# Performance work log

Hardware: AMD Instinct MI355X
Metric: run time of the kernel (lower is better)

The kernel has to match this reference:

```python
import jax, jax.numpy as jnp
import numpy as np
from jax import lax

HIDDEN = 1024; HEADS = 16; HEAD = 64; LAYERS = 4; MLP = 4096
PATCH = 16; TUBE = 2; CROP = 224; FRAMES = 16
GRID = CROP // PATCH          # 14
DEPTH = FRAMES // TUBE        # 8
N_TOK = DEPTH * GRID * GRID   # 1568
EPS = 1e-6
D_ROT = 2 * ((HEAD // 3) // 2)  # 20 per rotary axis (d, h, w); 4 dims left unrotated


def setup_inputs() -> dict:
    key = jax.random.key(0)
    ks = jax.random.split(key, 12)
    w = lambda k, shape: jax.random.normal(k, shape, jnp.float32) * 0.02
    L, H, M = LAYERS, HIDDEN, MLP
    return {
        "pixel_values_videos": jax.random.normal(ks[0], (2, FRAMES, 3, CROP, CROP), jnp.float32),
        "patch_w": w(ks[1], (H, 3, TUBE, PATCH, PATCH)),  # Conv3d OIDHW
        "patch_b": jnp.zeros((H,), jnp.float32),
        "ln1_g": jnp.ones((L, H), jnp.float32), "ln1_b": jnp.zeros((L, H), jnp.float32),
        "qw": w(ks[2], (L, H, H)), "qb": jnp.zeros((L, H), jnp.float32),
        "kw": w(ks[3], (L, H, H)), "kb": jnp.zeros((L, H), jnp.float32),
        "vw": w(ks[4], (L, H, H)), "vb": jnp.zeros((L, H), jnp.float32),
        "pw": w(ks[5], (L, H, H)), "pb": jnp.zeros((L, H), jnp.float32),
        "ln2_g": jnp.ones((L, H), jnp.float32), "ln2_b": jnp.zeros((L, H), jnp.float32),
        "fc1w": w(ks[6], (L, M, H)), "fc1b": jnp.zeros((L, M), jnp.float32),
        "fc2w": w(ks[7], (L, H, M)), "fc2b": jnp.zeros((L, H), jnp.float32),
        "lnf_g": jnp.ones((H,), jnp.float32), "lnf_b": jnp.zeros((H,), jnp.float32),
    }


def _layer_norm(x, g, b):
    mu = jnp.mean(x, axis=-1, keepdims=True)
    var = jnp.mean(jnp.square(x - mu), axis=-1, keepdims=True)
    return (x - mu) * lax.rsqrt(var + EPS) * g + b


def _position_ids():
    ids = jnp.arange(N_TOK)
    tpf = GRID * GRID
    d_pos = ids // tpf
    rem = ids - d_pos * tpf
    h_pos = rem // GRID
    w_pos = rem - h_pos * GRID
    return d_pos, h_pos, w_pos


def _rotate(x, pos):
    # x: (B, H, N, D); matches VJEPA2 rotate_queries_or_keys:
    # tiled (not interleaved) sin/cos * interleaved rotate-half.
    D = x.shape[-1]
    omega = 1.0 / (10000.0 ** (jnp.arange(D // 2, dtype=x.dtype) / (D / 2.0)))
    freq = pos.astype(x.dtype)[:, None] * omega              # (N, D/2)
    sin = jnp.concatenate([jnp.sin(freq)] * 2, axis=-1)      # (N, D) tiled (torch .repeat)
    cos = jnp.concatenate([jnp.cos(freq)] * 2, axis=-1)
    y = x.reshape(x.shape[:-1] + (D // 2, 2))
    y = jnp.stack([-y[..., 1], y[..., 0]], axis=-1).reshape(x.shape)
    return x * cos + y * sin


def _apply_rope(x, pos_ids):
    d_pos, h_pos, w_pos = pos_ids
    s0, s1, s2 = 0, D_ROT, 2 * D_ROT
    parts = [_rotate(x[..., s0:s1], d_pos), _rotate(x[..., s1:s2], h_pos),
             _rotate(x[..., s2:3 * D_ROT], w_pos)]
    if 3 * D_ROT < HEAD:
        parts.append(x[..., 3 * D_ROT:])
    return jnp.concatenate(parts, axis=-1)


def _forward(pixel_values_videos, patch_w, patch_b, ln1_g, ln1_b, qw, qb, kw, kb,
             vw, vb, pw, pb, ln2_g, ln2_b, fc1w, fc1b, fc2w, fc2b, lnf_g, lnf_b):
    B = pixel_values_videos.shape[0]
    x = jnp.transpose(pixel_values_videos, (0, 2, 1, 3, 4))  # (B, C, T, H, W)
    h = lax.conv_general_dilated(x, patch_w, window_strides=(TUBE, PATCH, PATCH),
                                 padding="VALID",
                                 dimension_numbers=("NCDHW", "OIDHW", "NCDHW"))
    h = h + patch_b[None, :, None, None, None]
    h = h.reshape(B, HIDDEN, -1).transpose(0, 2, 1)          # (B, N, HIDDEN)

    pos_ids = _position_ids()
    scale = HEAD ** -0.5

    for i in range(LAYERS):
        # attention block
        xn = _layer_norm(h, ln1_g[i], ln1_b[i])
        def heads(w_, b_):
            return (xn @ w_.T + b_).reshape(B, N_TOK, HEADS, HEAD).transpose(0, 2, 1, 3)
        q = _apply_rope(heads(qw[i], qb[i]), pos_ids)
        k = _apply_rope(heads(kw[i], kb[i]), pos_ids)
        v = heads(vw[i], vb[i])
        aw = jnp.einsum("bhnd,bhmd->bhnm", q, k) * scale
        aw = jax.nn.softmax(aw.astype(jnp.float32), axis=-1).astype(q.dtype)
        o = jnp.einsum("bhnm,bhmd->bhnd", aw, v)
        o = o.transpose(0, 2, 1, 3).reshape(B, N_TOK, HIDDEN)
        h = h + (o @ pw[i].T + pb[i])
        # MLP block
        xn = _layer_norm(h, ln2_g[i], ln2_b[i])
        m = jax.nn.gelu(xn @ fc1w[i].T + fc1b[i], approximate=False)
        h = h + (m @ fc2w[i].T + fc2b[i])

    return _layer_norm(h, lnf_g, lnf_b)


def reference(pixel_values_videos, patch_w, patch_b, ln1_g, ln1_b, qw, qb, kw, kb,
              vw, vb, pw, pb, ln2_g, ln2_b, fc1w, fc1b, fc2w, fc2b, lnf_g, lnf_b):
    return _forward(pixel_values_videos, patch_w, patch_b, ln1_g, ln1_b, qw, qb, kw, kb,
                    vw, vb, pw, pb, ln2_g, ln2_b, fc1w, fc1b, fc2w, fc2b, lnf_g, lnf_b)
```

## Files before the change

kernel.cpp:

```cpp
#include <hip/hip_runtime.h>
#include <math.h>

#define NTOK   1568
#define BATCH  2
#define HID    1024
#define MLPD   4096
#define NLAYER 4
#define ROWS   (BATCH*NTOK)
#define CONVK  1536

typedef __bf16 bf16x8 __attribute__((ext_vector_type(8)));
typedef __bf16 bf16x2 __attribute__((ext_vector_type(2)));
typedef float  f32x4  __attribute__((ext_vector_type(4)));

__device__ __forceinline__ unsigned short f2b(float f) {
  unsigned int u = __float_as_uint(f);
  unsigned int r = u + 0x7FFFu + ((u >> 16) & 1u);
  return (unsigned short)(r >> 16);
}
__device__ __forceinline__ float b2f(unsigned short s) {
  return __uint_as_float((unsigned int)s << 16);
}
__device__ __forceinline__ unsigned cvt2(float a, float b) {
  bf16x2 t;
  t[0] = (__bf16)a;
  t[1] = (__bf16)b;
  return __builtin_bit_cast(unsigned, t);
}
__device__ __forceinline__ float e2(float x) { return __builtin_amdgcn_exp2f(x); }

__device__ __forceinline__ void async16(const unsigned short* g, unsigned short* l) {
  __builtin_amdgcn_global_load_lds(
      (__attribute__((address_space(1))) void*)(void*)g,
      (__attribute__((address_space(3))) void*)(void*)l, 16, 0, 0);
}

__global__ __launch_bounds__(256) void cast4_k(const float* __restrict__ s,
                                               unsigned short* __restrict__ d,
                                               long long n4) {
  long long i = (long long)blockIdx.x * 256 + threadIdx.x;
  long long stride = (long long)gridDim.x * 256;
  for (; i < n4; i += stride) {
    float4 v = ((const float4*)s)[i];
    *(ushort4*)(d + i * 4) = make_ushort4(f2b(v.x), f2b(v.y), f2b(v.z), f2b(v.w));
  }
}

__global__ __launch_bounds__(256) void castqkv_k(const float* __restrict__ q,
                                                 const float* __restrict__ k,
                                                 const float* __restrict__ v,
                                                 unsigned short* __restrict__ dst) {
  const float* src = blockIdx.y == 0 ? q : (blockIdx.y == 1 ? k : v);
  long long i4 = (long long)blockIdx.x * 256 + threadIdx.x;
  long long e = i4 * 4;
  int layer = (int)(e >> 20);
  long long de = e + ((long long)(2 * layer + blockIdx.y) << 20);
  float4 val = ((const float4*)src)[i4];
  *(ushort4*)(dst + de) = make_ushort4(f2b(val.x), f2b(val.y), f2b(val.z), f2b(val.w));
}

__global__ __launch_bounds__(256) void biascat_k(const float* __restrict__ qb,
                                                 const float* __restrict__ kb,
                                                 const float* __restrict__ vb,
                                                 float* __restrict__ dst) {
  int idx = blockIdx.x * 256 + threadIdx.x;
  int layer = idx / 3072, c = idx % 3072;
  float v = c < 1024 ? qb[layer * 1024 + c]
            : (c < 2048 ? kb[layer * 1024 + c - 1024] : vb[layer * 1024 + c - 2048]);
  dst[idx] = v;
}

__global__ __launch_bounds__(256) void im2col_k(const float* __restrict__ pv,
                                                unsigned short* __restrict__ A) {
  int idx = blockIdx.x * 256 + threadIdx.x;
  int row = idx / CONVK, col = idx % CONVK;
  int b = row / NTOK, t = row % NTOK;
  int d = t / 196, r = t % 196, hh = r / 14, ww = r % 14;
  int c = col >> 9, r2 = col & 511, td = r2 >> 8, ph = (r2 >> 4) & 15, pw = r2 & 15;
  int frame = 2 * d + td;
  const float* src = pv + ((((long long)b * 16 + frame) * 3 + c) * 224 + (hh * 16 + ph)) * 224
                        + (ww * 16 + pw);
  A[idx] = f2b(*src);
}

__global__ __launch_bounds__(256) void gemm_bt(const unsigned short* __restrict__ A,
                                               const unsigned short* __restrict__ B,
                                               unsigned short* outP,
                                               int M, int N, int K, int kChunk,
                                               size_t zStride) {
  __shared__ unsigned short As[2][128 * 32];
  __shared__ unsigned short Bs[2][128 * 32];
  const int tid = threadIdx.x;
  const int lane = tid & 63;
  const int w = tid >> 6;
  const int wm = (w >> 1) * 64, wn = (w & 1) * 64;
  const int l15 = lane & 15, l4 = lane >> 4;
  const int bm = blockIdx.y, bn = blockIdx.x;
  const int wbase = tid & ~63;
  const int kbeg = blockIdx.z * kChunk;

  auto stage = [&](int buf, int k0) {
#pragma unroll
    for (int it = 0; it < 2; ++it) {
      int c = it * 256 + tid;
      int rowA = bm * 128 + (c >> 2);
      if (rowA >= M) rowA = M - 1;
      async16(A + (size_t)rowA * K + k0 + (c & 3) * 8, &As[buf][(it * 256 + wbase) * 8]);
      int rowB = bn * 128 + (c >> 2);
      async16(B + (size_t)rowB * K + k0 + (c & 3) * 8, &Bs[buf][(it * 256 + wbase) * 8]);
    }
  };

  f32x4 acc[4][4] = {};
  stage(0, kbeg);
  const int nIter = kChunk >> 5;

  for (int i = 0; i < nIter; ++i) {
    const int cur = i & 1;
    __syncthreads();
    if (i + 1 < nIter) stage(cur ^ 1, kbeg + (i + 1) * 32);

    bf16x8 af[4], bfr[4];
#pragma unroll
    for (int ii = 0; ii < 4; ++ii)
      af[ii] = *(const bf16x8*)&As[cur][(wm + ii * 16 + l15) * 32 + l4 * 8];
#pragma unroll
    for (int j = 0; j < 4; ++j)
      bfr[j] = *(const bf16x8*)&Bs[cur][(wn + j * 16 + l15) * 32 + l4 * 8];
#pragma unroll
    for (int ii = 0; ii < 4; ++ii)
#pragma unroll
      for (int j = 0; j < 4; ++j)
        acc[ii][j] = __builtin_amdgcn_mfma_f32_16x16x32_bf16(af[ii], bfr[j], acc[ii][j], 0, 0, 0);
  }

  unsigned short* pout = outP + (size_t)blockIdx.z * zStride;
#pragma unroll
  for (int ii = 0; ii < 4; ++ii) {
    int rowb = bm * 128 + wm + ii * 16 + l4 * 4;
#pragma unroll
    for (int r = 0; r < 4; ++r) {
      int rr = rowb + r;
      if (rr >= M) continue;
#pragma unroll
      for (int j = 0; j < 4; ++j) {
        int col = bn * 128 + wn + j * 16 + l15;
        pout[(size_t)rr * N + col] = f2b(acc[ii][j][r]);
      }
    }
  }
}

template <int NP, int GELU>
__global__ __launch_bounds__(256) void reduceN_k(const unsigned short* p,
                                                 const float* __restrict__ bias,
                                                 unsigned short* outB,
                                                 int MN, int N, size_t pStride) {
  int i8 = blockIdx.x * 256 + threadIdx.x;
  int e = i8 * 8;
  float acc[8];
#pragma unroll
  for (int j = 0; j < 8; ++j) acc[j] = 0.0f;
#pragma unroll
  for (int pp = 0; pp < NP; ++pp) {
    const unsigned short* src = p + (size_t)pp * pStride + e;
    ushort4 a0 = *(const ushort4*)src;
    ushort4 a1 = *(const ushort4*)(src + 4);
    acc[0] += b2f(a0.x); acc[1] += b2f(a0.y); acc[2] += b2f(a0.z); acc[3] += b2f(a0.w);
    acc[4] += b2f(a1.x); acc[5] += b2f(a1.y); acc[6] += b2f(a1.z); acc[7] += b2f(a1.w);
  }
  int col = e % N;
  float4 b0 = *(const float4*)(bias + col);
  float4 b1 = *(const float4*)(bias + col + 4);
  acc[0] += b0.x; acc[1] += b0.y; acc[2] += b0.z; acc[3] += b0.w;
  acc[4] += b1.x; acc[5] += b1.y; acc[6] += b1.z; acc[7] += b1.w;
  if (GELU) {
#pragma unroll
    for (int j = 0; j < 8; ++j)
      acc[j] = 0.5f * acc[j] * (1.0f + erff(acc[j] * 0.70710678118654752f));
  }
  *(ushort4*)(outB + e) = make_ushort4(f2b(acc[0]), f2b(acc[1]), f2b(acc[2]), f2b(acc[3]));
  *(ushort4*)(outB + e + 4) = make_ushort4(f2b(acc[4]), f2b(acc[5]), f2b(acc[6]), f2b(acc[7]));
}

template <int NP, int RESID, int FINAL>
__global__ __launch_bounds__(256) void redln_k(const unsigned short* __restrict__ p,
                                               const float* __restrict__ bias,
                                               const float* resid,
                                               const float* __restrict__ g,
                                               const float* __restrict__ b,
                                               float* hOut,
                                               unsigned short* __restrict__ xnOut,
                                               float* __restrict__ fOut,
                                               size_t pStride) {
  __shared__ float red[8];
  const int row = blockIdx.x, tid = threadIdx.x;
  const int col = tid * 4;
  const size_t off = (size_t)row * HID + col;
  float v0 = 0, v1 = 0, v2 = 0, v3 = 0;
#pragma unroll
  for (int pp = 0; pp < NP; ++pp) {
    ushort4 a = *(const ushort4*)(p + (size_t)pp * pStride + off);
    v0 += b2f(a.x); v1 += b2f(a.y); v2 += b2f(a.z); v3 += b2f(a.w);
  }
  float4 bs = *(const float4*)(bias + col);
  v0 += bs.x; v1 += bs.y; v2 += bs.z; v3 += bs.w;
  if (RESID) {
    float4 r = *(const float4*)(resid + off);
    v0 += r.x; v1 += r.y; v2 += r.z; v3 += r.w;
  }
  if (!FINAL) *(float4*)(hOut + off) = make_float4(v0, v1, v2, v3);
  float s = v0 + v1 + v2 + v3;
  float q = v0 * v0 + v1 * v1 + v2 * v2 + v3 * v3;
  for (int o2 = 32; o2; o2 >>= 1) { s += __shfl_xor(s, o2); q += __shfl_xor(q, o2); }
  if ((tid & 63) == 0) { red[tid >> 6] = s; red[4 + (tid >> 6)] = q; }
  __syncthreads();
  float ts = red[0] + red[1] + red[2] + red[3];
  float tq = red[4] + red[5] + red[6] + red[7];
  float mu = ts * (1.0f / HID);
  float var = tq * (1.0f / HID) - mu * mu;
  float rs = rsqrtf(var + 1e-6f);
  float o0 = (v0 - mu) * rs * g[col + 0] + b[col + 0];
  float o1 = (v1 - mu) * rs * g[col + 1] + b[col + 1];
  float o2 = (v2 - mu) * rs * g[col + 2] + b[col + 2];
  float o3 = (v3 - mu) * rs * g[col + 3] + b[col + 3];
  if (FINAL) {
    *(float4*)(fOut + off) = make_float4(o0, o1, o2, o3);
  } else {
    *(ushort4*)(xnOut + off) = make_ushort4(f2b(o0), f2b(o1), f2b(o2), f2b(o3));
  }
}

__global__ __launch_bounds__(256) void qkvprep_k(const unsigned short* __restrict__ qkvb,
                                                 unsigned short* __restrict__ Qh,
                                                 unsigned short* __restrict__ Kh,
                                                 unsigned short* __restrict__ VT) {
  __shared__ unsigned short Vs[64 * 72];
  const int tile = blockIdx.x, bh = blockIdx.y;
  const int b = bh >> 4, head = bh & 15;
  const int tid = threadIdx.x;
  const int tl = tid >> 2, dc = tid & 3;
  const int tg = tile * 64 + tl;
  const int trc = tg < NTOK ? tg : NTOK - 1;
  const bool valid = tg < NTOK;
  const size_t srow = ((size_t)(b * NTOK + trc)) * 3072 + head * 64 + dc * 16;

  {
    uint4 v0 = *(const uint4*)(qkvb + srow + 2048);
    uint4 v1 = *(const uint4*)(qkvb + srow + 2048 + 8);
    *(uint4*)&Vs[tl * 72 + dc * 16] = v0;
    *(uint4*)&Vs[tl * 72 + dc * 16 + 8] = v1;
  }

  const int t = trc;
  const int dpos = t / 196, rem = t - dpos * 196, hpos = rem / 14, wpos = rem - hpos * 14;
  const float LG = 0.9210340371976184f;
  union V16 { uint4 u[2]; unsigned short s[16]; };
  V16 qin, kin, qout, kout;
  qin.u[0] = *(const uint4*)(qkvb + srow);
  qin.u[1] = *(const uint4*)(qkvb + srow + 8);
  kin.u[0] = *(const uint4*)(qkvb + srow + 1024);
  kin.u[1] = *(const uint4*)(qkvb + srow + 1024 + 8);
#pragma unroll
  for (int p = 0; p < 8; ++p) {
    int d0 = dc * 16 + 2 * p;
    float qx0 = b2f(qin.s[2 * p]), qx1 = b2f(qin.s[2 * p + 1]);
    float kx0 = b2f(kin.s[2 * p]), kx1 = b2f(kin.s[2 * p + 1]);
    float qo0, qo1, ko0, ko1;
    if (d0 >= 60) { qo0 = qx0; qo1 = qx1; ko0 = kx0; ko1 = kx1; }
    else {
      int region = d0 / 20;
      int j0 = d0 - region * 20;
      int pos = region == 0 ? dpos : (region == 1 ? hpos : wpos);
      float fp = (float)pos;
      int i0 = j0 % 10, i1 = (j0 + 1) % 10;
      float f0 = expf(-LG * (float)i0) * fp;
      float f1 = expf(-LG * (float)i1) * fp;
      float c0 = cosf(f0), s0 = sinf(f0), c1 = cosf(f1), s1 = sinf(f1);
      qo0 = qx0 * c0 - qx1 * s0; qo1 = qx1 * c1 + qx0 * s1;
      ko0 = kx0 * c0 - kx1 * s0; ko1 = kx1 * c1 + kx0 * s1;
    }
    const float QS = 0.18033688011112042f;
    qout.s[2 * p]     = f2b(qo0 * QS);
    qout.s[2 * p + 1] = f2b(qo1 * QS);
    kout.s[2 * p]     = f2b(ko0);
    kout.s[2 * p + 1] = f2b(ko1);
  }
  if (valid) {
    size_t drow = ((size_t)bh * NTOK + tg) * 64 + dc * 16;
    *(uint4*)(Qh + drow)     = qout.u[0];
    *(uint4*)(Qh + drow + 8) = qout.u[1];
    *(uint4*)(Kh + drow)     = kout.u[0];
    *(uint4*)(Kh + drow + 8) = kout.u[1];
  }
  __syncthreads();
  {
    int d = tid >> 2, tc = tid & 3;
    if (tile * 64 + tc * 16 < NTOK) {
      V16 o;
#pragma unroll
      for (int jj = 0; jj < 16; ++jj) o.s[jj] = Vs[(tc * 16 + jj) * 72 + d];
      unsigned short* dst = VT + ((size_t)bh * 64 + d) * NTOK + tile * 64 + tc * 16;
      *(uint4*)dst = o.u[0];
      *(uint4*)(dst + 8) = o.u[1];
    }
  }
}

__global__ __launch_bounds__(256, 4) void flash5_k(const unsigned short* __restrict__ Qh,
                                                   const unsigned short* __restrict__ Kh,
                                                   const unsigned short* __restrict__ VT,
                                                   unsigned short* __restrict__ Opart,
                                                   float2* __restrict__ ml) {
  __shared__ unsigned short Ks[2][64 * 64];
  __shared__ unsigned short Vs[2][64 * 64];
  const int bh = blockIdx.x, qt = blockIdx.y, kv = blockIdx.z;
  const int kt0 = kv ? 13 : 0, kt1 = kv ? 25 : 13;
  const int tid = threadIdx.x, lane = tid & 63, w = tid >> 6;
  const int l15 = lane & 15, l4 = lane >> 4;
  const size_t hb = (size_t)bh * NTOK * 64;
  const unsigned short* kgp = Kh + hb;
  const unsigned short* vbp = VT + (size_t)bh * 64 * NTOK;

  const int srow0 = w * 8 + (lane >> 3);
  const int scg0  = (lane & 7) ^ (srow0 & 7);
  const int srow1 = srow0 + 32;
  const int scg1  = (lane & 7) ^ (srow1 & 7);

  const int qrow = qt * 64 + w * 16 + l15;
  const int qrc = qrow < NTOK ? qrow : NTOK - 1;
  bf16x8 q0 = *(const bf16x8*)(Qh + hb + (size_t)qrc * 64 + l4 * 8);
  bf16x8 q1 = *(const bf16x8*)(Qh + hb + (size_t)qrc * 64 + 32 + l4 * 8);

  f32x4 oacc[4] = {};
  float m = -1e30f, l = 0.0f;

  {
    const int kc0 = kt0 * 64;
    async16(kgp + (size_t)(kc0 + srow0) * 64 + scg0 * 8, &Ks[0][(size_t)w * 512]);
    async16(kgp + (size_t)(kc0 + srow1) * 64 + scg1 * 8, &Ks[0][(size_t)(w + 4) * 512]);
    async16(vbp + (size_t)srow0 * NTOK + kc0 + scg0 * 8, &Vs[0][(size_t)w * 512]);
    async16(vbp + (size_t)srow1 * NTOK + kc0 + scg1 * 8, &Vs[0][(size_t)(w + 4) * 512]);
  }

  const int h7 = l15 & 7;
  const int p1 = (l4 ^ h7) * 8;
  const int p2 = ((l4 + 4) ^ h7) * 8;

  for (int kt = kt0; kt < kt1; ++kt) {
    const int cur = (kt - kt0) & 1, nxt = cur ^ 1;
    const int kb = kt * 64;
    __syncthreads();

    if (kt + 1 < kt1) {
      const int kn = kb + 64;
      async16(kgp + (size_t)(kn + srow0) * 64 + scg0 * 8, &Ks[nxt][(size_t)w * 512]);
      async16(kgp + (size_t)(kn + srow1) * 64 + scg1 * 8, &Ks[nxt][(size_t)(w + 4) * 512]);
      async16(vbp + (size_t)srow0 * NTOK + kn + scg0 * 8, &Vs[nxt][(size_t)w * 512]);
      async16(vbp + (size_t)srow1 * NTOK + kn + scg1 * 8, &Vs[nxt][(size_t)(w + 4) * 512]);
    }

    bf16x8 kc0[4], kc1[4];
#pragma unroll
    for (int nt = 0; nt < 4; ++nt) {
      const unsigned short* kr = &Ks[cur][(nt * 16 + l15) * 64];
      kc0[nt] = *(const bf16x8*)(kr + p1);
      kc1[nt] = *(const bf16x8*)(kr + p2);
    }
    f32x4 s[4] = {};
    __builtin_amdgcn_s_setprio(1);
#pragma unroll
    for (int nt = 0; nt < 4; ++nt) {
      s[nt] = __builtin_amdgcn_mfma_f32_16x16x32_bf16(kc0[nt], q0, s[nt], 0, 0, 0);
      s[nt] = __builtin_amdgcn_mfma_f32_16x16x32_bf16(kc1[nt], q1, s[nt], 0, 0, 0);
    }
    __builtin_amdgcn_s_setprio(0);
    bf16x8 vf0[4], vf1[4];
#pragma unroll
    for (int dt = 0; dt < 4; ++dt) {
      const unsigned short* vr = &Vs[cur][(dt * 16 + l15) * 64];
      vf0[dt] = *(const bf16x8*)(vr + p1);
      vf1[dt] = *(const bf16x8*)(vr + p2);
    }

    if (kb + 64 > NTOK) {
#pragma unroll
      for (int nt = 0; nt < 4; ++nt)
#pragma unroll
        for (int r = 0; r < 4; ++r)
          if (kb + nt * 16 + l4 * 4 + r >= NTOK) s[nt][r] = -1e30f;
    }
    float rmax = s[0][0];
#pragma unroll
    for (int nt = 0; nt < 4; ++nt)
#pragma unroll
      for (int r = 0; r < 4; ++r) rmax = fmaxf(rmax, s[nt][r]);
    rmax = fmaxf(rmax, __shfl_xor(rmax, 16));
    rmax = fmaxf(rmax, __shfl_xor(rmax, 32));
    if (!__all(rmax - m <= 11.5f)) {
      float mn = fmaxf(m, rmax);
      float alpha = e2(m - mn);
      m = mn;
      l *= alpha;
#pragma unroll
      for (int dt = 0; dt < 4; ++dt)
#pragma unroll
        for (int r = 0; r < 4; ++r) oacc[dt][r] *= alpha;
    }
    float rsum = 0.0f;
#pragma unroll
    for (int nt = 0; nt < 4; ++nt)
#pragma unroll
      for (int r = 0; r < 4; ++r) {
        float p = e2(s[nt][r] - m);
        s[nt][r] = p;
        rsum += p;
      }
    rsum += __shfl_xor(rsum, 16);
    rsum += __shfl_xor(rsum, 32);
    l += rsum;

    unsigned pk01[4], pk23[4];
#pragma unroll
    for (int nt = 0; nt < 4; ++nt) {
      pk01[nt] = cvt2(s[nt][0], s[nt][1]);
      pk23[nt] = cvt2(s[nt][2], s[nt][3]);
    }
    const int srcA = ((l4 & 1) << 5) | l15;
    const int srcB = srcA + 16;
    const bool hi = (l4 >> 1) != 0;
    union PB { unsigned u[4]; bf16x8 v; } pf[2];
#pragma unroll
    for (int kc = 0; kc < 2; ++kc) {
      unsigned t0, t1;
      t0 = __shfl(pk01[2 * kc], srcA); t1 = __shfl(pk01[2 * kc + 1], srcA);
      pf[kc].u[0] = hi ? t1 : t0;
      t0 = __shfl(pk23[2 * kc], srcA); t1 = __shfl(pk23[2 * kc + 1], srcA);
      pf[kc].u[1] = hi ? t1 : t0;
      t0 = __shfl(pk01[2 * kc], srcB); t1 = __shfl(pk01[2 * kc + 1], srcB);
      pf[kc].u[2] = hi ? t1 : t0;
      t0 = __shfl(pk23[2 * kc], srcB); t1 = __shfl(pk23[2 * kc + 1], srcB);
      pf[kc].u[3] = hi ? t1 : t0;
    }
    __builtin_amdgcn_s_setprio(1);
#pragma unroll
    for (int dt = 0; dt < 4; ++dt) {
      oacc[dt] = __builtin_amdgcn_mfma_f32_16x16x32_bf16(vf0[dt], pf[0].v, oacc[dt], 0, 0, 0);
      oacc[dt] = __builtin_amdgcn_mfma_f32_16x16x32_bf16(vf1[dt], pf[1].v, oacc[dt], 0, 0, 0);
    }
    __builtin_amdgcn_s_setprio(0);
  }

  __syncthreads();
  unsigned short* Os = &Ks[0][0];
#pragma unroll
  for (int dt = 0; dt < 4; ++dt)
#pragma unroll
    for (int r = 0; r < 4; ++r)
      Os[w * 1152 + l15 * 72 + dt * 16 + l4 * 4 + r] = f2b(oacc[dt][r]);
  if (qrow < NTOK) {
    uint4 a  = *(const uint4*)&Os[w * 1152 + l15 * 72 + l4 * 16];
    uint4 bq = *(const uint4*)&Os[w * 1152 + l15 * 72 + l4 * 16 + 8];
    unsigned short* op = Opart + ((size_t)(kv * 32 + bh) * NTOK + qrow) * 64;
    *(uint4*)(op + l4 * 16) = a;
    *(uint4*)(op + l4 * 16 + 8) = bq;
    if (l4 == 0) ml[(size_t)(kv * 32 + bh) * NTOK + qrow] = make_float2(m, l);
  }
}

__global__ __launch_bounds__(256) void fcomb_k(const unsigned short* __restrict__ Op,
                                               const float2* __restrict__ ml,
                                               unsigned short* __restrict__ O) {
  const int bh = blockIdx.x, qt = blockIdx.y;
  const int tid = threadIdx.x;
  const int qr = qt * 64 + (tid >> 2);
  const int dc = (tid & 3) * 16;
  if (qr >= NTOK) return;
  const int b = bh >> 4, head = bh & 15;
  float2 a0 = ml[(size_t)bh * NTOK + qr];
  float2 a1 = ml[(size_t)(32 + bh) * NTOK + qr];
  float M = fmaxf(a0.x, a1.x);
  float w0 = e2(a0.x - M), w1 = e2(a1.x - M);
  float inv = 1.0f / (a0.y * w0 + a1.y * w1);
  w0 *= inv; w1 *= inv;
  union V16 { uint4 u[2]; unsigned short s[16]; } p0, p1, o;
  const unsigned short* q0 = Op + ((size_t)bh * NTOK + qr) * 64 + dc;
  const unsigned short* q1 = Op + ((size_t)(32 + bh) * NTOK + qr) * 64 + dc;
  p0.u[0] = *(const uint4*)q0;       p0.u[1] = *(const uint4*)(q0 + 8);
  p1.u[0] = *(const uint4*)q1;       p1.u[1] = *(const uint4*)(q1 + 8);
#pragma unroll
  for (int j = 0; j < 16; ++j) o.s[j] = f2b(b2f(p0.s[j]) * w0 + b2f(p1.s[j]) * w1);
  unsigned short* dst = O + ((size_t)(b * NTOK + qr)) * HID + head * 64 + dc;
  *(uint4*)dst = o.u[0];
  *(uint4*)(dst + 8) = o.u[1];
}

extern "C" void kernel_launch(void* const* d_in, const int* in_sizes, int n_in,
                              void* d_out, int out_size, void* d_ws, size_t ws_size,
                              hipStream_t stream) {
  (void)in_sizes; (void)n_in; (void)out_size; (void)ws_size;
  const float* pv      = (const float*)d_in[0];
  const float* patch_w = (const float*)d_in[1];
  const float* patch_b = (const float*)d_in[2];
  const float* ln1_g   = (const float*)d_in[3];
  const float* ln1_b   = (const float*)d_in[4];
  const float* qw = (const float*)d_in[5];
  const float* qb = (const float*)d_in[6];
  const float* kw = (const float*)d_in[7];
  const float* kb = (const float*)d_in[8];
  const float* vw = (const float*)d_in[9];
  const float* vb = (const float*)d_in[10];
  const float* pw = (const float*)d_in[11];
  const float* pb = (const float*)d_in[12];
  const float* ln2_g = (const float*)d_in[13];
  const float* ln2_b = (const float*)d_in[14];
  const float* fc1w = (const float*)d_in[15];
  const float* fc1b = (const float*)d_in[16];
  const float* fc2w = (const float*)d_in[17];
  const float* fc2b = (const float*)d_in[18];
  const float* lnf_g = (const float*)d_in[19];
  const float* lnf_b = (const float*)d_in[20];

  char* wsp = (char*)d_ws;
  auto alloc = [&](size_t bytes) {
    char* p = wsp;
    wsp += (bytes + 255) & ~(size_t)255;
    return p;
  };
  unsigned short* wPatch = (unsigned short*)alloc((size_t)1024 * 1536 * 2);
  unsigned short* wQKV   = (unsigned short*)alloc((size_t)NLAYER * 3072 * 1024 * 2);
  unsigned short* wP     = (unsigned short*)alloc((size_t)NLAYER * HID * HID * 2);
  unsigned short* wF1    = (unsigned short*)alloc((size_t)NLAYER * MLPD * HID * 2);
  unsigned short* wF2    = (unsigned short*)alloc((size_t)NLAYER * HID * MLPD * 2);
  float*          qkvbias = (float*)alloc((size_t)NLAYER * 3072 * 4);
  unsigned short* Aim  = (unsigned short*)alloc((size_t)ROWS * CONVK * 2);
  float*          h    = (float*)alloc((size_t)ROWS * HID * 4);
  unsigned short* xnb  = (unsigned short*)alloc((size_t)ROWS * HID * 2);
  unsigned short* qkvo = (unsigned short*)alloc((size_t)ROWS * 3072 * 2);
  unsigned short* Qh   = (unsigned short*)alloc((size_t)ROWS * HID * 2 + 8192);
  unsigned short* Kh   = (unsigned short*)alloc((size_t)ROWS * HID * 2 + 8192);
  unsigned short* VT   = (unsigned short*)alloc((size_t)ROWS * HID * 2 + 8192);
  unsigned short* ob   = (unsigned short*)alloc((size_t)ROWS * HID * 2);
  unsigned short* mb   = (unsigned short*)alloc((size_t)ROWS * MLPD * 2);

  unsigned short* part  = Qh;
  unsigned short* partM = mb;
  unsigned short* Opart = mb;
  float2*         mlbuf = (float2*)(mb + (size_t)2 * 32 * NTOK * 64);
  const size_t MNs = (size_t)ROWS * HID;
  const size_t strideF1 = (size_t)(mb - part);

  auto cast = [&](const float* s, unsigned short* d, long long n) {
    long long n4 = n / 4;
    int grid = (int)((n4 + 255) / 256);
    if (grid > 16384) grid = 16384;
    cast4_k<<<grid, 256, 0, stream>>>(s, d, n4);
  };
  cast(patch_w, wPatch, (long long)1024 * 1536);
  castqkv_k<<<dim3(4096, 3), 256, 0, stream>>>(qw, kw, vw, wQKV);
  cast(pw, wP, (long long)NLAYER * HID * HID);
  cast(fc1w, wF1, (long long)NLAYER * MLPD * HID);
  cast(fc2w, wF2, (long long)NLAYER * HID * MLPD);
  biascat_k<<<48, 256, 0, stream>>>(qb, kb, vb, qkvbias);

  im2col_k<<<(ROWS * CONVK) / 256, 256, 0, stream>>>(pv, Aim);
  gemm_bt<<<dim3(8, 25, 3), 256, 0, stream>>>(Aim, wPatch, part, ROWS, HID, CONVK, 512, MNs);
  redln_k<3, 0, 0><<<ROWS, 256, 0, stream>>>(
      part, patch_b, nullptr, ln1_g, ln1_b, h, xnb, nullptr, MNs);

  for (int i = 0; i < NLAYER; ++i) {
    gemm_bt<<<dim3(24, 25, 2), 256, 0, stream>>>(
        xnb, wQKV + (size_t)i * 3072 * 1024, part, ROWS, 3072, HID, 512,
        (size_t)ROWS * 3072);
    reduceN_k<2, 0><<<(ROWS * 3072) / 2048, 256, 0, stream>>>(
        part, qkvbias + i * 3072, qkvo, ROWS * 3072, 3072, (size_t)ROWS * 3072);
    qkvprep_k<<<dim3(25, 32), 256, 0, stream>>>(qkvo, Qh, Kh, VT);
    flash5_k<<<dim3(32, 25, 2), 256, 0, stream>>>(Qh, Kh, VT, Opart, mlbuf);
    fcomb_k<<<dim3(32, 25), 256, 0, stream>>>(Opart, mlbuf, ob);
    gemm_bt<<<dim3(8, 25, 4), 256, 0, stream>>>(
        ob, wP + (size_t)i * HID * HID, partM, ROWS, HID, HID, 256, MNs);
    redln_k<4, 1, 0><<<ROWS, 256, 0, stream>>>(
        partM, pb + i * HID, h, ln2_g + i * HID, ln2_b + i * HID, h, xnb, nullptr, MNs);
    gemm_bt<<<dim3(32, 25, 2), 256, 0, stream>>>(
        xnb, wF1 + (size_t)i * MLPD * HID, part, ROWS, MLPD, HID, 512, strideF1);
    reduceN_k<2, 1><<<(ROWS * MLPD) / 2048, 256, 0, stream>>>(
        part, fc1b + i * MLPD, mb, ROWS * MLPD, MLPD, strideF1);
    gemm_bt<<<dim3(8, 25, 4), 256, 0, stream>>>(
        mb, wF2 + (size_t)i * HID * MLPD, part, ROWS, HID, MLPD, 1024, MNs);
    if (i < NLAYER - 1) {
      redln_k<4, 1, 0><<<ROWS, 256, 0, stream>>>(
          part, fc2b + i * HID, h, ln1_g + (i + 1) * HID, ln1_b + (i + 1) * HID,
          h, xnb, nullptr, MNs);
    } else {
      redln_k<4, 1, 1><<<ROWS, 256, 0, stream>>>(
          part, fc2b + i * HID, h, lnf_g, lnf_b, nullptr, nullptr, (float*)d_out, MNs);
    }
  }
}
```

Baseline: 1.390 ms.

## Triple-buffer GEMM staging with swizzled LDS layout and explicit vmcnt waits

The bf16 GEMM moves from double to triple LDS buffering, prefetching two K-steps ahead and replacing __syncthreads with an explicit vmcnt wait plus s_barrier, so global loads have more time to land. The 16-byte chunks within each row are XOR-swizzled by row to reduce LDS bank conflicts on the fragment reads. The MFMA block also gets raised wave priority and scheduling barriers. The extra buffer raises LDS use per block, which may lower occupancy. Correctness depends on the hand-counted vmcnt value matching the number of outstanding async loads.

```diff
diff --git a/kernel.cpp b/kernel.cpp
--- a/kernel.cpp
+++ b/kernel.cpp
@@ -88,8 +88,8 @@
                                                unsigned short* outP,
                                                int M, int N, int K, int kChunk,
                                                size_t zStride) {
-  __shared__ unsigned short As[2][128 * 32];
-  __shared__ unsigned short Bs[2][128 * 32];
+  __shared__ unsigned short As[3][128 * 32];
+  __shared__ unsigned short Bs[3][128 * 32];
   const int tid = threadIdx.x;
   const int lane = tid & 63;
   const int w = tid >> 6;
@@ -103,35 +103,52 @@
 #pragma unroll
     for (int it = 0; it < 2; ++it) {
       int c = it * 256 + tid;
-      int rowA = bm * 128 + (c >> 2);
+      int row = c >> 2;
+      int sc = (c & 3) ^ ((row >> 1) & 3);
+      int rowA = bm * 128 + row;
       if (rowA >= M) rowA = M - 1;
-      async16(A + (size_t)rowA * K + k0 + (c & 3) * 8, &As[buf][(it * 256 + wbase) * 8]);
-      int rowB = bn * 128 + (c >> 2);
-      async16(B + (size_t)rowB * K + k0 + (c & 3) * 8, &Bs[buf][(it * 256 + wbase) * 8]);
+      async16(A + (size_t)rowA * K + k0 + sc * 8, &As[buf][(it * 256 + wbase) * 8]);
+      int rowB = bn * 128 + row;
+      async16(B + (size_t)rowB * K + k0 + sc * 8, &Bs[buf][(it * 256 + wbase) * 8]);
     }
   };
 
   f32x4 acc[4][4] = {};
+  const int nIter = kChunk >> 5;
+
   stage(0, kbeg);
-  const int nIter = kChunk >> 5;
-
+  stage(1, kbeg + 32);
+
+  const int pchunk = (l4 ^ ((l15 >> 1) & 3)) * 8;
+
+  int cur = 0, pre = 2;
   for (int i = 0; i < nIter; ++i) {
-    const int cur = i & 1;
-    __syncthreads();
-    if (i + 1 < nIter) stage(cur ^ 1, kbeg + (i + 1) * 32);
+    if (i + 1 < nIter) {
+      asm volatile("s_waitcnt vmcnt(4)" ::: "memory");
+    } else {
+      asm volatile("s_waitcnt vmcnt(0)" ::: "memory");
+    }
+    __builtin_amdgcn_s_barrier();
+    __builtin_amdgcn_sched_barrier(0);
+    if (i + 2 < nIter) stage(pre, kbeg + (i + 2) * 32);
 
     bf16x8 af[4], bfr[4];
 #pragma unroll
     for (int ii = 0; ii < 4; ++ii)
-      af[ii] = *(const bf16x8*)&As[cur][(wm + ii * 16 + l15) * 32 + l4 * 8];
+      af[ii] = *(const bf16x8*)&As[cur][(wm + ii * 16 + l15) * 32 + pchunk];
 #pragma unroll
     for (int j = 0; j < 4; ++j)
-      bfr[j] = *(const bf16x8*)&Bs[cur][(wn + j * 16 + l15) * 32 + l4 * 8];
+      bfr[j] = *(const bf16x8*)&Bs[cur][(wn + j * 16 + l15) * 32 + pchunk];
+    __builtin_amdgcn_s_setprio(1);
 #pragma unroll
     for (int ii = 0; ii < 4; ++ii)
 #pragma unroll
       for (int j = 0; j < 4; ++j)
         acc[ii][j] = __builtin_amdgcn_mfma_f32_16x16x32_bf16(af[ii], bfr[j], acc[ii][j], 0, 0, 0);
+    __builtin_amdgcn_s_setprio(0);
+    __builtin_amdgcn_sched_barrier(0);
+    cur = cur == 2 ? 0 : cur + 1;
+    pre = pre == 2 ? 0 : pre + 1;
   }
 
   unsigned short* pout = outP + (size_t)blockIdx.z * zStride;
```

New measurement: 1.392 ms. No clear change (+0.2%).
